# Optimization experiments

Measured on AMD Instinct MI355X. Metric: run time of the kernel, lower is better.

Reference implementation:

```python
import jax, jax.numpy as jnp
import numpy as np

NFMODES = 512   # spinful lattice: 2 * 256 sites
NE = 256        # number of occupied fermion modes per configuration
NUNPAIRED = 32
NMODES = NFMODES - NUNPAIRED
BATCH = 32


def slogpf(A):
    """(sign, log|Pf|) of an even-dim antisymmetric matrix via Parlett-Reid
    LTL^T elimination with partial pivoting (pfapack pfaffian_LTL algorithm)."""
    n = A.shape[0]
    ar = jnp.arange(n)
    one = jnp.asarray(1.0, A.dtype)
    zero = jnp.asarray(0.0, A.dtype)

    def step(carry, k):
        A, sign, logabs = carry
        # pivot row: argmax |A[k+1:, k]|
        m1 = ar > k
        kp = jnp.argmax(jnp.where(m1, jnp.abs(A[:, k]), -one))
        # swap rows and columns k+1 <-> kp (Pf flips sign on a swap)
        perm = ar.at[k + 1].set(kp).at[kp].set(k + 1)
        A = A[perm][:, perm]
        sign = jnp.where(kp != k + 1, -sign, sign)
        pivot = A[k, k + 1]  # Pf *= A[k, k+1]
        sign = sign * jnp.sign(pivot)
        logabs = logabs + jnp.log(jnp.abs(pivot))
        # rank-2 update of the trailing submatrix A[k+2:, k+2:]
        m2 = ar > (k + 1)
        tau = jnp.where(m2, A[k, :] / pivot, zero)  # A[k, k+2:] / A[k, k+1]
        c = jnp.where(m2, A[:, k + 1], zero)        # A[k+2:, k+1]
        A = A + jnp.outer(tau, c) - jnp.outer(c, tau)
        return (A, sign, logabs), None

    ks = jnp.arange(0, n - 1, 2)
    (_, sign, logabs), _ = jax.lax.scan(step, (A, one, zero), ks)
    return sign, logabs


def setup_inputs() -> dict:
    key = jax.random.key(0)
    k1, k2, k3 = jax.random.split(key, 3)
    U = jax.random.normal(k1, (NFMODES, NFMODES), jnp.float32)
    # equal-pairing diagonal init (as in the module) + noise for nontrivial pivoting
    diag = jnp.diag(jnp.tile(jnp.array([1.0, 0.0], jnp.float32), NMODES // 2)[:-1], k=1)
    J = diag + 0.1 * jax.random.normal(k2, (NMODES, NMODES), jnp.float32)
    # occupied-mode indices: NE unique sorted indices per sample (fermion_idx output)
    idx = jax.vmap(lambda k: jnp.sort(jax.random.permutation(k, NFMODES)[:NE]))(
        jax.random.split(k3, BATCH)).astype(jnp.int32)
    return {"U": U, "J": J, "idx": idx, "Nunpaired": NUNPAIRED}


def reference(U, J, idx, Nunpaired):
    Ja = (J - J.T) / 2  # enforce antisymmetry of the pairing matrix

    def single(ix):
        Usel = U[ix]                      # [NE, NFMODES] gather of occupied rows
        Uun = Usel[:, :Nunpaired]         # [NE, Nunpaired] unpaired orbitals
        Up = Usel[:, Nunpaired:]          # [NE, NMODES]   paired orbitals
        F = Up @ Ja @ Up.T                # [NE, NE] antisymmetric pairing block
        O = jnp.zeros((Nunpaired, Nunpaired), F.dtype)
        Ffull = jnp.block([[F, Uun], [-Uun.T, O]])  # [NE+Nun, NE+Nun]
        return slogpf(Ffull)

    sign, logabs = jax.vmap(single)(idx)
    return sign, logabs
```

## Files before the change

kernel.cpp:

```cpp
#include <hip/hip_runtime.h>
#include <hip/hip_bf16.h>
#include <math.h>

#define NFM 512
#define NE  256
#define NUN 32
#define NM  480
#define NB  32
#define NF  288
#define WP  16
#define PAIRS 8
#define PP  18
#define THETA 0.03125f

typedef unsigned long long ull;

__global__ __launch_bounds__(256)
void gemm_w_k(const float* __restrict__ U, const float* __restrict__ J,
              float* __restrict__ W) {
  const int m0 = blockIdx.y << 6;
  const int n0 = blockIdx.x << 6;
  const int tid = threadIdx.x;
  __shared__ float As[16][64];
  __shared__ float Bs[16][64];
  const int ar = tid >> 2, ac = (tid & 3) << 2;
  const int br = tid >> 4, bc = (tid & 15) << 2;
  const int tx = tid & 15, ty = tid >> 4;
  const float* Arow = U + (size_t)(m0 + ar) * NFM + NUN;
  float acc[4][4] = {};
  for (int l0 = 0; l0 < NM; l0 += 16) {
    float4 av = *(const float4*)(Arow + l0 + ac);
    As[ac + 0][ar] = av.x; As[ac + 1][ar] = av.y;
    As[ac + 2][ar] = av.z; As[ac + 3][ar] = av.w;
    {
      const int kk = l0 + br;
      float4 bj = make_float4(0.f, 0.f, 0.f, 0.f);
      if (n0 + bc < NM) {
        float4 jr = *(const float4*)(J + (size_t)kk * NM + n0 + bc);
        float t0 = J[(size_t)(n0 + bc + 0) * NM + kk];
        float t1 = J[(size_t)(n0 + bc + 1) * NM + kk];
        float t2 = J[(size_t)(n0 + bc + 2) * NM + kk];
        float t3 = J[(size_t)(n0 + bc + 3) * NM + kk];
        bj = make_float4(0.5f * (jr.x - t0), 0.5f * (jr.y - t1),
                         0.5f * (jr.z - t2), 0.5f * (jr.w - t3));
      }
      *(float4*)(&Bs[br][bc]) = bj;
    }
    __syncthreads();
#pragma unroll
    for (int kk = 0; kk < 16; ++kk) {
      float4 a4 = *(const float4*)(&As[kk][ty << 2]);
      float4 b4 = *(const float4*)(&Bs[kk][tx << 2]);
      float a[4] = {a4.x, a4.y, a4.z, a4.w};
      float bb[4] = {b4.x, b4.y, b4.z, b4.w};
#pragma unroll
      for (int q = 0; q < 4; ++q)
#pragma unroll
        for (int p = 0; p < 4; ++p) acc[q][p] = fmaf(a[q], bb[p], acc[q][p]);
    }
    __syncthreads();
  }
#pragma unroll
  for (int q = 0; q < 4; ++q) {
    int r = m0 + (ty << 2) + q;
#pragma unroll
    for (int p = 0; p < 4; ++p) {
      int m = n0 + (tx << 2) + p;
      if (m < NM) W[(size_t)r * NM + m] = acc[q][p];
    }
  }
}

__global__ __launch_bounds__(256)
void gemm2_k(const float* __restrict__ U, const int* __restrict__ idx,
             const float* __restrict__ W, float* __restrict__ Ff) {
  const int b  = blockIdx.z;
  const int by = blockIdx.y, bx = blockIdx.x;
  if (bx == 4) {
    if (by != 0) return;
    const int tid = threadIdx.x;
    float* Fb = Ff + (size_t)b * NF * NF;
    const int gr = idx[b * NE + tid];
#pragma unroll 4
    for (int u = 0; u < NUN; ++u) {
      float v = U[(size_t)gr * NFM + u];
      Fb[(size_t)tid * NF + NE + u] = v;
      Fb[(size_t)(NE + u) * NF + tid] = -v;
    }
    if (tid < NUN) {
      for (int v = 0; v < NUN; ++v) Fb[(size_t)(NE + tid) * NF + NE + v] = 0.f;
    }
    return;
  }
  if (by < bx) return;
  const int m0 = by << 6;
  const int n0 = bx << 6;
  const int tid = threadIdx.x;
  __shared__ float As[16][64];
  __shared__ float Bs[16][64];
  const int ar = tid >> 2, ac = (tid & 3) << 2;
  const int jr = tid >> 2, kc = (tid & 3) << 2;
  const int tx = tid & 15, ty = tid >> 4;
  const float* Arow = W + (size_t)idx[b * NE + m0 + ar] * NM;
  const float* Brow = U + (size_t)idx[b * NE + n0 + jr] * NFM + NUN;
  float acc[4][4] = {};
  for (int l0 = 0; l0 < NM; l0 += 16) {
    float4 av = *(const float4*)(Arow + l0 + ac);
    As[ac + 0][ar] = av.x; As[ac + 1][ar] = av.y;
    As[ac + 2][ar] = av.z; As[ac + 3][ar] = av.w;
    float4 bv = *(const float4*)(Brow + l0 + kc);
    Bs[kc + 0][jr] = bv.x; Bs[kc + 1][jr] = bv.y;
    Bs[kc + 2][jr] = bv.z; Bs[kc + 3][jr] = bv.w;
    __syncthreads();
#pragma unroll
    for (int kk = 0; kk < 16; ++kk) {
      float4 a4 = *(const float4*)(&As[kk][ty << 2]);
      float4 b4 = *(const float4*)(&Bs[kk][tx << 2]);
      float a[4] = {a4.x, a4.y, a4.z, a4.w};
      float bb[4] = {b4.x, b4.y, b4.z, b4.w};
#pragma unroll
      for (int q = 0; q < 4; ++q)
#pragma unroll
        for (int p = 0; p < 4; ++p) acc[q][p] = fmaf(a[q], bb[p], acc[q][p]);
    }
    __syncthreads();
  }
  float* Fb = Ff + (size_t)b * NF * NF;
  const bool mirror = (by > bx);
#pragma unroll
  for (int q = 0; q < 4; ++q) {
    int i = m0 + (ty << 2) + q;
#pragma unroll
    for (int p = 0; p < 4; ++p) {
      int j = n0 + (tx << 2) + p;
      Fb[(size_t)i * NF + j] = acc[q][p];
      if (mirror) Fb[(size_t)j * NF + i] = -acc[q][p];
    }
  }
}

__global__ __launch_bounds__(512)
void pfpanel_k(float* __restrict__ Ff, float* __restrict__ out) {
  const int b = blockIdx.x;
  float* __restrict__ A = Ff + (size_t)b * NF * NF;
  const int tid = threadIdx.x;
  __shared__ __align__(16) float P[NF * PP];
  __shared__ __align__(16) float2 s_tc[PAIRS][NF];
  __shared__ __align__(16) float s_colbuf[NF];
  __shared__ float s_oldrow[WP];
  __shared__ float s_pivdef[2];
  __shared__ float s_invp[PAIRS];
  __shared__ __align__(16) unsigned s_redu[2][8];

  float sign = 1.f, logabs = 0.f;

#pragma unroll 1
  for (int k0 = 0; k0 < NF; k0 += WP) {
    const int pend = k0 + WP;

    if (k0 == 0) {
      for (int e = tid; e < NF * 4; e += 512) {
        int r = e >> 2, c4 = (e & 3) << 2;
        float4 v = *(const float4*)(A + (size_t)r * NF + c4);
        float2* d = (float2*)&P[r * PP + c4];
        d[0] = make_float2(v.x, v.y);
        d[1] = make_float2(v.z, v.w);
      }
      __syncthreads();
    }

#pragma unroll 1
    for (int mp = 0; mp < PAIRS; ++mp) {
      const int k = k0 + 2 * mp, lc = 2 * mp, lc1 = lc + 1;
      const int par = mp & 1;

      float vk = 0.f, vk1 = 0.f;
      unsigned pk = 0;
      if (tid > k && tid < NF) {
        float2 pv = *(const float2*)&P[tid * PP + lc];
        vk = pv.x; vk1 = pv.y;
#pragma unroll
        for (int m = 0; m < PAIRS - 1; ++m) {
          float2 ti  = s_tc[m][tid];
          float2 tk  = s_tc[m][k];
          float2 tk1 = s_tc[m][k + 1];
          float im = s_invp[m];
          float d0 = im * (ti.x * tk.y  - ti.y * tk.x);
          float d1 = im * (ti.x * tk1.y - ti.y * tk1.x);
          vk  += (m < mp) ? d0 : 0.f;
          vk1 += (m < mp) ? d1 : 0.f;
        }
        s_colbuf[tid] = vk;
        if (tid > k + 1) s_tc[mp][tid] = make_float2(-vk, vk1);
        else             s_pivdef[par] = vk;
        pk = (__float_as_uint(fabsf(vk)) & 0xFFFFFE00u) | (unsigned)tid;
      }
#pragma unroll
      for (int s = 32; s > 0; s >>= 1) {
        unsigned o = (unsigned)__shfl_xor((int)pk, s, 64);
        if (o > pk) pk = o;
      }
      if ((tid & 63) == 0) s_redu[par][tid >> 6] = pk;
      __syncthreads();
      uint4 r0 = *(const uint4*)&s_redu[par][0];
      uint4 r1 = *(const uint4*)&s_redu[par][4];
      unsigned best = r0.x;
      best = best > r0.y ? best : r0.y;
      best = best > r0.z ? best : r0.z;
      best = best > r0.w ? best : r0.w;
      best = best > r1.x ? best : r1.x;
      best = best > r1.y ? best : r1.y;
      best = best > r1.z ? best : r1.z;
      best = best > r1.w ? best : r1.w;
      const float vmax = __uint_as_float(best & 0xFFFFFE00u);
      const float pivdef = -s_pivdef[par];
      const bool doswap = fabsf(pivdef) < THETA * vmax;

      if (!doswap) {
        const float invp = 1.f / pivdef;
        s_invp[mp] = invp;
        if (tid == 0) {
          sign *= (pivdef > 0.f ? 1.f : (pivdef < 0.f ? -1.f : 0.f));
          logabs += logf(fabsf(pivdef));
        }
      } else {
        const int kp = (int)(best & 0x1FFu);
        const float pivot = -s_colbuf[kp];
        const float invp = 1.f / pivot;
        s_invp[mp] = invp;
        if (tid == 0) {
          sign = -sign;
          sign *= (pivot > 0.f ? 1.f : (pivot < 0.f ? -1.f : 0.f));
          logabs += logf(fabsf(pivot));
        }
        const bool inpanel = (kp < pend);
        float gvr = 0.f;
        if (inpanel) {
          const int lckp = kp - k0;
          if (tid > k + 1 && tid < NF && tid != kp) {
            float a = P[tid * PP + lc1], b2 = P[tid * PP + lckp];
            P[tid * PP + lc1] = b2; P[tid * PP + lckp] = a;
          } else if (tid >= NF && tid < NF + WP) {
            int c = tid - NF;
            if (c != lc1 && c != lckp) {
              float a = P[(k + 1) * PP + c], b2 = P[kp * PP + c];
              P[(k + 1) * PP + c] = b2; P[kp * PP + c] = a;
            }
          } else if (tid == NF + WP) {
            float a = P[kp * PP + lc1];
            float b2 = P[(k + 1) * PP + lckp];
            P[(k + 1) * PP + lc1] = 0.f;  P[(k + 1) * PP + lckp] = a;
            P[kp * PP + lc1] = b2;        P[kp * PP + lckp] = 0.f;
          } else if (tid >= NF + 24 && tid < NF + 24 + mp) {
            int m = tid - (NF + 24);
            float2 a = s_tc[m][k + 1], b2 = s_tc[m][kp];
            s_tc[m][k + 1] = b2; s_tc[m][kp] = a;
          }
        } else {
          if (tid >= pend && tid < NF) {
            if (tid == kp) {
              A[(size_t)kp * NF + kp] = 0.f;
            } else {
              float pvv = P[tid * PP + lc1];
              gvr = A[(size_t)tid * NF + kp];
              A[(size_t)tid * NF + kp] = pvv;
              A[(size_t)kp * NF + tid] = -pvv;
            }
          } else if (tid >= NF && tid < NF + WP) {
            int c = tid - NF;
            float old = P[kp * PP + c];
            s_oldrow[c] = old;
            P[kp * PP + c] = P[(k + 1) * PP + c];
          } else if (tid >= NF + 24 && tid < NF + 24 + mp) {
            int m = tid - (NF + 24);
            float2 a = s_tc[m][k + 1], b2 = s_tc[m][kp];
            s_tc[m][k + 1] = b2; s_tc[m][kp] = a;
          }
        }
        __syncthreads();
        if (tid > k + 1 && tid < NF) {
          float vpost = (tid == kp) ? s_colbuf[k + 1] : vk;
          float cc;
          if (inpanel)        cc = P[tid * PP + lc1];
          else if (tid < pend) cc = -s_oldrow[tid - k0];
          else if (tid == kp)  cc = -s_oldrow[lc1];
          else                 cc = gvr;
#pragma unroll 1
          for (int m = 0; m < mp; ++m) {
            const float im = s_invp[m];
            float2 ti = s_tc[m][tid], tk1 = s_tc[m][k + 1];
            cc = fmaf(ti.x, im * tk1.y, fmaf(-ti.y, im * tk1.x, cc));
          }
          s_tc[mp][tid] = make_float2(-vpost, cc);
        }
        __syncthreads();
      }
    }
    __syncthreads();

    if (pend < NF) {
      const int ty = tid >> 6, tx = tid & 63;
      const int nch = (NF - pend) >> 2;
      float ivr[PAIRS];
#pragma unroll
      for (int m = 0; m < PAIRS; ++m) ivr[m] = s_invp[m];
      for (int jb = 0; jb < nch; jb += 64) {
        const int j4 = jb + tx;
        if (j4 < nch) {
          const int j = pend + (j4 << 2);
          const bool stageP = (j4 < (WP >> 2));
          float4 tj[PAIRS], cj[PAIRS];
#pragma unroll
          for (int m = 0; m < PAIRS; ++m) {
            const float im = ivr[m];
            float4 q0 = *(const float4*)(&s_tc[m][j]);
            float4 q1 = *(const float4*)(&s_tc[m][j + 2]);
            tj[m] = make_float4(q0.x * im, q0.z * im, q1.x * im, q1.z * im);
            cj[m] = make_float4(q0.y * im, q0.w * im, q1.y * im, q1.w * im);
          }
#pragma unroll 2
          for (int i = pend + ty; i < NF; i += 8) {
            float* ap = A + (size_t)i * NF + j;
            float4 a = *(float4*)ap;
#pragma unroll
            for (int m = 0; m < PAIRS; ++m) {
              const float2 t = s_tc[m][i];
              a.x = fmaf(t.x, cj[m].x, fmaf(-t.y, tj[m].x, a.x));
              a.y = fmaf(t.x, cj[m].y, fmaf(-t.y, tj[m].y, a.y));
              a.z = fmaf(t.x, cj[m].z, fmaf(-t.y, tj[m].z, a.z));
              a.w = fmaf(t.x, cj[m].w, fmaf(-t.y, tj[m].w, a.w));
            }
            *(float4*)ap = a;
            if (stageP) {
              float2* d = (float2*)&P[i * PP + (j - pend)];
              d[0] = make_float2(a.x, a.y);
              d[1] = make_float2(a.z, a.w);
            }
          }
        }
      }
    }
    __syncthreads();
  }

  if (tid == 0) { out[b] = sign; out[NB + b] = logabs; }
}

extern "C" void kernel_launch(void* const* d_in, const int* in_sizes, int n_in,
                              void* d_out, int out_size, void* d_ws, size_t ws_size,
                              hipStream_t stream) {
  const float* U  = (const float*)d_in[0];
  const float* J  = (const float*)d_in[1];
  const int* idx  = (const int*)d_in[2];
  float* out = (float*)d_out;
  float* ws = (float*)d_ws;

  float* W  = ws;
  float* Ff = W + (size_t)NFM * NM;

  gemm_w_k<<<dim3(8, 8), dim3(256), 0, stream>>>(U, J, W);
  gemm2_k<<<dim3(5, 4, NB), dim3(256), 0, stream>>>(U, idx, W, Ff);
  pfpanel_k<<<dim3(NB), dim3(512), 0, stream>>>(Ff, out);
}
```

Measured before the change: 337.9 us.

## Pack two batch samples per 1024-thread block in Pfaffian panel kernel

The Pfaffian kernel now processes two batch matrices per workgroup of 1024 threads, with each 512-thread half owning its own shared-memory buffers. Because __syncthreads spans both halves, the swap decision is unified: the swap path is taken if either sample needs a pivot swap, with per-half guards. This halves the number of workgroups to 16 on a GPU with many CUs, so more work sits on each CU. It risks lower overall parallelism and extra synchronization coupling between the two samples.

```diff
diff --git a/kernel.cpp b/kernel.cpp
--- a/kernel.cpp
+++ b/kernel.cpp
@@ -12,6 +12,7 @@
 #define PAIRS 8
 #define PP  18
 #define THETA 0.03125f
+#define NH  512
 
 typedef unsigned long long ull;
 
@@ -139,18 +140,20 @@
   }
 }
 
-__global__ __launch_bounds__(512)
+__global__ __launch_bounds__(1024)
 void pfpanel_k(float* __restrict__ Ff, float* __restrict__ out) {
-  const int b = blockIdx.x;
+  const int tid = threadIdx.x;
+  const int sub = tid >> 9;
+  const int stid = tid & (NH - 1);
+  const int b = (blockIdx.x << 1) | sub;
   float* __restrict__ A = Ff + (size_t)b * NF * NF;
-  const int tid = threadIdx.x;
-  __shared__ __align__(16) float P[NF * PP];
-  __shared__ __align__(16) float2 s_tc[PAIRS][NF];
-  __shared__ __align__(16) float s_colbuf[NF];
-  __shared__ float s_oldrow[WP];
-  __shared__ float s_pivdef[2];
-  __shared__ float s_invp[PAIRS];
-  __shared__ __align__(16) unsigned s_redu[2][8];
+  __shared__ __align__(16) float P[2][NF * PP];
+  __shared__ __align__(16) float2 s_tc[2][PAIRS][NF];
+  __shared__ __align__(16) float s_colbuf[2][NF];
+  __shared__ float s_oldrow[2][WP];
+  __shared__ float s_pivdef[2][2];
+  __shared__ float s_invp[2][PAIRS];
+  __shared__ __align__(16) unsigned s_redu[2][2][8];
 
   float sign = 1.f, logabs = 0.f;
 
@@ -159,10 +162,10 @@
     const int pend = k0 + WP;
 
     if (k0 == 0) {
-      for (int e = tid; e < NF * 4; e += 512) {
+      for (int e = stid; e < NF * 4; e += NH) {
         int r = e >> 2, c4 = (e & 3) << 2;
         float4 v = *(const float4*)(A + (size_t)r * NF + c4);
-        float2* d = (float2*)&P[r * PP + c4];
+        float2* d = (float2*)&P[sub][r * PP + c4];
         d[0] = make_float2(v.x, v.y);
         d[1] = make_float2(v.z, v.w);
       }
@@ -176,34 +179,34 @@
 
       float vk = 0.f, vk1 = 0.f;
       unsigned pk = 0;
-      if (tid > k && tid < NF) {
-        float2 pv = *(const float2*)&P[tid * PP + lc];
+      if (stid > k && stid < NF) {
+        float2 pv = *(const float2*)&P[sub][stid * PP + lc];
         vk = pv.x; vk1 = pv.y;
 #pragma unroll
         for (int m = 0; m < PAIRS - 1; ++m) {
-          float2 ti  = s_tc[m][tid];
-          float2 tk  = s_tc[m][k];
-          float2 tk1 = s_tc[m][k + 1];
-          float im = s_invp[m];
+          float2 ti  = s_tc[sub][m][stid];
+          float2 tk  = s_tc[sub][m][k];
+          float2 tk1 = s_tc[sub][m][k + 1];
+          float im = s_invp[sub][m];
           float d0 = im * (ti.x * tk.y  - ti.y * tk.x);
           float d1 = im * (ti.x * tk1.y - ti.y * tk1.x);
           vk  += (m < mp) ? d0 : 0.f;
           vk1 += (m < mp) ? d1 : 0.f;
         }
-        s_colbuf[tid] = vk;
-        if (tid > k + 1) s_tc[mp][tid] = make_float2(-vk, vk1);
-        else             s_pivdef[par] = vk;
-        pk = (__float_as_uint(fabsf(vk)) & 0xFFFFFE00u) | (unsigned)tid;
+        s_colbuf[sub][stid] = vk;
+        if (stid > k + 1) s_tc[sub][mp][stid] = make_float2(-vk, vk1);
+        else              s_pivdef[sub][par] = vk;
+        pk = (__float_as_uint(fabsf(vk)) & 0xFFFFFE00u) | (unsigned)stid;
       }
 #pragma unroll
       for (int s = 32; s > 0; s >>= 1) {
         unsigned o = (unsigned)__shfl_xor((int)pk, s, 64);
         if (o > pk) pk = o;
       }
-      if ((tid & 63) == 0) s_redu[par][tid >> 6] = pk;
+      if ((stid & 63) == 0) s_redu[sub][par][stid >> 6] = pk;
       __syncthreads();
-      uint4 r0 = *(const uint4*)&s_redu[par][0];
-      uint4 r1 = *(const uint4*)&s_redu[par][4];
+      uint4 r0 = *(const uint4*)&s_redu[sub][par][0];
+      uint4 r1 = *(const uint4*)&s_redu[sub][par][4];
       unsigned best = r0.x;
       best = best > r0.y ? best : r0.y;
       best = best > r0.z ? best : r0.z;
@@ -213,85 +216,112 @@
       best = best > r1.z ? best : r1.z;
       best = best > r1.w ? best : r1.w;
       const float vmax = __uint_as_float(best & 0xFFFFFE00u);
-      const float pivdef = -s_pivdef[par];
+      const float pivdef = -s_pivdef[sub][par];
       const bool doswap = fabsf(pivdef) < THETA * vmax;
-
-      if (!doswap) {
+      uint4 o0 = *(const uint4*)&s_redu[sub ^ 1][par][0];
+      uint4 o1 = *(const uint4*)&s_redu[sub ^ 1][par][4];
+      unsigned bestO = o0.x;
+      bestO = bestO > o0.y ? bestO : o0.y;
+      bestO = bestO > o0.z ? bestO : o0.z;
+      bestO = bestO > o0.w ? bestO : o0.w;
+      bestO = bestO > o1.x ? bestO : o1.x;
+      bestO = bestO > o1.y ? bestO : o1.y;
+      bestO = bestO > o1.z ? bestO : o1.z;
+      bestO = bestO > o1.w ? bestO : o1.w;
+      const float vmaxO = __uint_as_float(bestO & 0xFFFFFE00u);
+      const float pivdefO = -s_pivdef[sub ^ 1][par];
+      const bool doswapO = fabsf(pivdefO) < THETA * vmaxO;
+      const bool anyswap = doswap || doswapO;
+
+      if (!anyswap) {
         const float invp = 1.f / pivdef;
-        s_invp[mp] = invp;
-        if (tid == 0) {
+        s_invp[sub][mp] = invp;
+        if (stid == 0) {
           sign *= (pivdef > 0.f ? 1.f : (pivdef < 0.f ? -1.f : 0.f));
           logabs += logf(fabsf(pivdef));
         }
       } else {
-        const int kp = (int)(best & 0x1FFu);
-        const float pivot = -s_colbuf[kp];
-        const float invp = 1.f / pivot;
-        s_invp[mp] = invp;
-        if (tid == 0) {
-          sign = -sign;
-          sign *= (pivot > 0.f ? 1.f : (pivot < 0.f ? -1.f : 0.f));
-          logabs += logf(fabsf(pivot));
-        }
-        const bool inpanel = (kp < pend);
+        int kp = k + 1;
+        bool inpanel = true;
+        if (!doswap) {
+          const float invp = 1.f / pivdef;
+          s_invp[sub][mp] = invp;
+          if (stid == 0) {
+            sign *= (pivdef > 0.f ? 1.f : (pivdef < 0.f ? -1.f : 0.f));
+            logabs += logf(fabsf(pivdef));
+          }
+        } else {
+          kp = (int)(best & 0x1FFu);
+          const float pivot = -s_colbuf[sub][kp];
+          const float invp = 1.f / pivot;
+          s_invp[sub][mp] = invp;
+          if (stid == 0) {
+            sign = -sign;
+            sign *= (pivot > 0.f ? 1.f : (pivot < 0.f ? -1.f : 0.f));
+            logabs += logf(fabsf(pivot));
+          }
+          inpanel = (kp < pend);
+        }
         float gvr = 0.f;
-        if (inpanel) {
-          const int lckp = kp - k0;
-          if (tid > k + 1 && tid < NF && tid != kp) {
-            float a = P[tid * PP + lc1], b2 = P[tid * PP + lckp];
-            P[tid * PP + lc1] = b2; P[tid * PP + lckp] = a;
-          } else if (tid >= NF && tid < NF + WP) {
-            int c = tid - NF;
-            if (c != lc1 && c != lckp) {
-              float a = P[(k + 1) * PP + c], b2 = P[kp * PP + c];
-              P[(k + 1) * PP + c] = b2; P[kp * PP + c] = a;
+        if (doswap) {
+          if (inpanel) {
+            const int lckp = kp - k0;
+            if (stid > k + 1 && stid < NF && stid != kp) {
+              float a = P[sub][stid * PP + lc1], b2 = P[sub][stid * PP + lckp];
+              P[sub][stid * PP + lc1] = b2; P[sub][stid * PP + lckp] = a;
+            } else if (stid >= NF && stid < NF + WP) {
+              int c = stid - NF;
+              if (c != lc1 && c != lckp) {
+                float a = P[sub][(k + 1) * PP + c], b2 = P[sub][kp * PP + c];
+                P[sub][(k + 1) * PP + c] = b2; P[sub][kp * PP + c] = a;
+              }
+            } else if (stid == NF + WP) {
+              float a = P[sub][kp * PP + lc1];
+              float b2 = P[sub][(k + 1) * PP + lckp];
+              P[sub][(k + 1) * PP + lc1] = 0.f;  P[sub][(k + 1) * PP + lckp] = a;
+              P[sub][kp * PP + lc1] = b2;        P[sub][kp * PP + lckp] = 0.f;
+            } else if (stid >= NF + 24 && stid < NF + 24 + mp) {
+              int m = stid - (NF + 24);
+              float2 a = s_tc[sub][m][k + 1], b2 = s_tc[sub][m][kp];
+              s_tc[sub][m][k + 1] = b2; s_tc[sub][m][kp] = a;
             }
-          } else if (tid == NF + WP) {
-            float a = P[kp * PP + lc1];
-            float b2 = P[(k + 1) * PP + lckp];
-            P[(k + 1) * PP + lc1] = 0.f;  P[(k + 1) * PP + lckp] = a;
-            P[kp * PP + lc1] = b2;        P[kp * PP + lckp] = 0.f;
-          } else if (tid >= NF + 24 && tid < NF + 24 + mp) {
-            int m = tid - (NF + 24);
-            float2 a = s_tc[m][k + 1], b2 = s_tc[m][kp];
-            s_tc[m][k + 1] = b2; s_tc[m][kp] = a;
-          }
-        } else {
-          if (tid >= pend && tid < NF) {
-            if (tid == kp) {
-              A[(size_t)kp * NF + kp] = 0.f;
-            } else {
-              float pvv = P[tid * PP + lc1];
-              gvr = A[(size_t)tid * NF + kp];
-              A[(size_t)tid * NF + kp] = pvv;
-              A[(size_t)kp * NF + tid] = -pvv;
+          } else {
+            if (stid >= pend && stid < NF) {
+              if (stid == kp) {
+                A[(size_t)kp * NF + kp] = 0.f;
+              } else {
+                float pvv = P[sub][stid * PP + lc1];
+                gvr = A[(size_t)stid * NF + kp];
+                A[(size_t)stid * NF + kp] = pvv;
+                A[(size_t)kp * NF + stid] = -pvv;
+              }
+            } else if (stid >= NF && stid < NF + WP) {
+              int c = stid - NF;
+              float old = P[sub][kp * PP + c];
+              s_oldrow[sub][c] = old;
+              P[sub][kp * PP + c] = P[sub][(k + 1) * PP + c];
+            } else if (stid >= NF + 24 && stid < NF + 24 + mp) {
+              int m = stid - (NF + 24);
+              float2 a = s_tc[sub][m][k + 1], b2 = s_tc[sub][m][kp];
+              s_tc[sub][m][k + 1] = b2; s_tc[sub][m][kp] = a;
             }
-          } else if (tid >= NF && tid < NF + WP) {
-            int c = tid - NF;
-            float old = P[kp * PP + c];
-            s_oldrow[c] = old;
-            P[kp * PP + c] = P[(k + 1) * PP + c];
-          } else if (tid >= NF + 24 && tid < NF + 24 + mp) {
-            int m = tid - (NF + 24);
-            float2 a = s_tc[m][k + 1], b2 = s_tc[m][kp];
-            s_tc[m][k + 1] = b2; s_tc[m][kp] = a;
           }
         }
         __syncthreads();
-        if (tid > k + 1 && tid < NF) {
-          float vpost = (tid == kp) ? s_colbuf[k + 1] : vk;
+        if (doswap && stid > k + 1 && stid < NF) {
+          float vpost = (stid == kp) ? s_colbuf[sub][k + 1] : vk;
           float cc;
-          if (inpanel)        cc = P[tid * PP + lc1];
-          else if (tid < pend) cc = -s_oldrow[tid - k0];
-          else if (tid == kp)  cc = -s_oldrow[lc1];
-          else                 cc = gvr;
+          if (inpanel)         cc = P[sub][stid * PP + lc1];
+          else if (stid < pend) cc = -s_oldrow[sub][stid - k0];
+          else if (stid == kp)  cc = -s_oldrow[sub][lc1];
+          else                  cc = gvr;
 #pragma unroll 1
           for (int m = 0; m < mp; ++m) {
-            const float im = s_invp[m];
-            float2 ti = s_tc[m][tid], tk1 = s_tc[m][k + 1];
+            const float im = s_invp[sub][m];
+            float2 ti = s_tc[sub][m][stid], tk1 = s_tc[sub][m][k + 1];
             cc = fmaf(ti.x, im * tk1.y, fmaf(-ti.y, im * tk1.x, cc));
           }
-          s_tc[mp][tid] = make_float2(-vpost, cc);
+          s_tc[sub][mp][stid] = make_float2(-vpost, cc);
         }
         __syncthreads();
       }
@@ -299,11 +329,11 @@
     __syncthreads();
 
     if (pend < NF) {
-      const int ty = tid >> 6, tx = tid & 63;
+      const int ty = stid >> 6, tx = stid & 63;
       const int nch = (NF - pend) >> 2;
       float ivr[PAIRS];
 #pragma unroll
-      for (int m = 0; m < PAIRS; ++m) ivr[m] = s_invp[m];
+      for (int m = 0; m < PAIRS; ++m) ivr[m] = s_invp[sub][m];
       for (int jb = 0; jb < nch; jb += 64) {
         const int j4 = jb + tx;
         if (j4 < nch) {
@@ -313,8 +343,8 @@
 #pragma unroll
           for (int m = 0; m < PAIRS; ++m) {
             const float im = ivr[m];
-            float4 q0 = *(const float4*)(&s_tc[m][j]);
-            float4 q1 = *(const float4*)(&s_tc[m][j + 2]);
+            float4 q0 = *(const float4*)(&s_tc[sub][m][j]);
+            float4 q1 = *(const float4*)(&s_tc[sub][m][j + 2]);
             tj[m] = make_float4(q0.x * im, q0.z * im, q1.x * im, q1.z * im);
             cj[m] = make_float4(q0.y * im, q0.w * im, q1.y * im, q1.w * im);
           }
@@ -324,7 +354,7 @@
             float4 a = *(float4*)ap;
 #pragma unroll
             for (int m = 0; m < PAIRS; ++m) {
-              const float2 t = s_tc[m][i];
+              const float2 t = s_tc[sub][m][i];
               a.x = fmaf(t.x, cj[m].x, fmaf(-t.y, tj[m].x, a.x));
               a.y = fmaf(t.x, cj[m].y, fmaf(-t.y, tj[m].y, a.y));
               a.z = fmaf(t.x, cj[m].z, fmaf(-t.y, tj[m].z, a.z));
@@ -332,7 +362,7 @@
             }
             *(float4*)ap = a;
             if (stageP) {
-              float2* d = (float2*)&P[i * PP + (j - pend)];
+              float2* d = (float2*)&P[sub][i * PP + (j - pend)];
               d[0] = make_float2(a.x, a.y);
               d[1] = make_float2(a.z, a.w);
             }
@@ -343,7 +373,7 @@
     __syncthreads();
   }
 
-  if (tid == 0) { out[b] = sign; out[NB + b] = logabs; }
+  if (stid == 0) { out[b] = sign; out[NB + b] = logabs; }
 }
 
 extern "C" void kernel_launch(void* const* d_in, const int* in_sizes, int n_in,
@@ -360,5 +390,5 @@
 
   gemm_w_k<<<dim3(8, 8), dim3(256), 0, stream>>>(U, J, W);
   gemm2_k<<<dim3(5, 4, NB), dim3(256), 0, stream>>>(U, idx, W, Ff);
-  pfpanel_k<<<dim3(NB), dim3(512), 0, stream>>>(Ff, out);
+  pfpanel_k<<<dim3(NB / 2), dim3(1024), 0, stream>>>(Ff, out);
 }
```

After: 481.8 us. +42.6%, slower.
